# Optimization experiments

Hardware: AMD Instinct MI355X
Metric: run time of the kernel (lower is better)

Reference implementation:

```python
import jax, jax.numpy as jnp
import numpy as np

N_NODES = 50000
N_EDGES = 800000
IN_FEAT = 100
OUT_FEAT = 100
NUM_RELS = 200
NUM_HEADS = 3
NUM_BASES = 100
SUB_IN = 1   # in_feat // num_bases
SUB_OUT = 1  # out_feat // num_bases


def setup_inputs() -> dict:
    key = jax.random.key(0)
    ks = jax.random.split(key, 10)
    return {
        "h": jax.random.normal(ks[0], (N_NODES, IN_FEAT), jnp.float32),
        "e": jax.random.normal(ks[1], (N_EDGES, IN_FEAT), jnp.float32),
        "norm": jax.random.uniform(ks[2], (N_NODES, 1), jnp.float32),
        "weight": jax.random.normal(ks[3], (NUM_RELS, NUM_BASES * SUB_IN * SUB_OUT), jnp.float32) * 0.1,
        "attn": jax.random.normal(ks[4], (NUM_RELS, NUM_HEADS, OUT_FEAT), jnp.float32) * 0.1,
        "fc_w": jax.random.normal(ks[5], (IN_FEAT, OUT_FEAT * NUM_HEADS), jnp.float32) * 0.1,
        "loop_w": jax.random.normal(ks[6], (IN_FEAT, OUT_FEAT), jnp.float32) * 0.1,
        "rel": jax.random.randint(ks[7], (N_EDGES,), 0, NUM_RELS, jnp.int32),
        "src": jax.random.randint(ks[8], (N_EDGES,), 0, N_NODES, jnp.int32),
        "dst": jax.random.randint(ks[9], (N_EDGES,), 0, N_NODES, jnp.int32),
    }


def reference(h, e, norm, weight, attn, fc_w, loop_w, rel, src, dst):
    E = rel.shape[0]
    # --- relation-indexed block-diagonal message (torch.bmm over blocks) ---
    W_e = weight[rel].reshape(E, NUM_BASES, SUB_IN, SUB_OUT)        # per-edge block weights
    h_src = h[src].reshape(E, NUM_BASES, SUB_IN)                    # gathered src features
    msg = jnp.einsum('ebi,ebio->ebo', h_src, W_e).reshape(E, OUT_FEAT)
    # --- edge-feature attention fuse ---
    a_e = attn[rel]                                                 # (E, H, OUT)
    fc_e = (e @ fc_w).reshape(E, NUM_HEADS, OUT_FEAT)               # fc(edge)
    feat = jax.nn.leaky_relu(a_e * fc_e, 0.2).sum(axis=1)           # (E, OUT)
    msg = msg + feat
    # --- scatter-sum aggregation to dst nodes, then norm + self-loop ---
    agg = jax.ops.segment_sum(msg, dst, num_segments=N_NODES)       # (N, OUT)
    node = agg * norm
    loop_message = h @ loop_w
    return node + loop_message
```

## Files before the change

### kernel.cpp

```cpp
#include <hip/hip_runtime.h>
#include <hip/hip_bf16.h>

#define N_NODES 50000
#define N_EDGES 800000
#define IN_FEAT 100
#define OUT_FEAT 100
#define NUM_RELS 200
#define NUM_HEADS 3

#define KP 128
#define NPH 112
#define NP  336
#define MB  128
#define NT_O 7

#define WS_B       0u
#define WS_LW      86016u
#define WS_CNT     114688u
#define WS_OFFS    315392u
#define WS_CURSOR  516096u
#define WS_BSUM    716800u
#define WS_PERM    717056u
#define WS_FEAT    3917056u
#define NNODES_PAD 50176

typedef __attribute__((ext_vector_type(8))) short short8;
typedef __attribute__((ext_vector_type(4))) float f32x4;

__device__ __forceinline__ unsigned short f2bf(float f) {
    unsigned u = __builtin_bit_cast(unsigned, f);
    unsigned r = u + 0x7FFFu + ((u >> 16) & 1u);
    return (unsigned short)(r >> 16);
}
__device__ __forceinline__ float bf2f(unsigned hs) {
    return __builtin_bit_cast(float, hs << 16);
}

__global__ __launch_bounds__(256) void build_B(const float* __restrict__ fc_w,
                                               unsigned short* __restrict__ Bws) {
    int idx = blockIdx.x * 256 + threadIdx.x;
    if (idx >= NP * 16) return;
    int n = idx >> 4, g = idx & 15;
    int head = n / NPH, nl = n - head * NPH;
    int kt = g >> 2, g4 = g & 3;
    unsigned p[4];
#pragma unroll
    for (int half = 0; half < 2; ++half) {
#pragma unroll
        for (int jp = 0; jp < 2; ++jp) {
            int k_lo = kt * 32 + half * 16 + g4 * 4 + jp * 2;
            int k_hi = k_lo + 1;
            float vlo = (k_lo < IN_FEAT && nl < OUT_FEAT)
                      ? fc_w[k_lo * (OUT_FEAT * NUM_HEADS) + head * OUT_FEAT + nl] : 0.f;
            float vhi = (k_hi < IN_FEAT && nl < OUT_FEAT)
                      ? fc_w[k_hi * (OUT_FEAT * NUM_HEADS) + head * OUT_FEAT + nl] : 0.f;
            p[half * 2 + jp] = (unsigned)f2bf(vlo) | ((unsigned)f2bf(vhi) << 16);
        }
    }
    unsigned off = (unsigned)(head * (NPH * KP * 2)) +
                   (((unsigned)(nl * (KP * 2) + g * 16)) ^ (((unsigned)(nl & 7)) << 4));
    *reinterpret_cast<int4*>(reinterpret_cast<char*>(Bws) + off) =
        make_int4((int)p[0], (int)p[1], (int)p[2], (int)p[3]);
}

__global__ __launch_bounds__(256) void build_LW(const float* __restrict__ loop_w,
                                                unsigned short* __restrict__ LWws) {
    int idx = blockIdx.x * 256 + threadIdx.x;
    if (idx >= NPH * 16) return;
    int nl = idx >> 4, g = idx & 15;
    int kt = g >> 2, g4 = g & 3;
    unsigned p[4];
#pragma unroll
    for (int half = 0; half < 2; ++half) {
#pragma unroll
        for (int jp = 0; jp < 2; ++jp) {
            int k_lo = kt * 32 + half * 16 + g4 * 4 + jp * 2;
            int k_hi = k_lo + 1;
            float vlo = (k_lo < IN_FEAT && nl < OUT_FEAT) ? loop_w[k_lo * OUT_FEAT + nl] : 0.f;
            float vhi = (k_hi < IN_FEAT && nl < OUT_FEAT) ? loop_w[k_hi * OUT_FEAT + nl] : 0.f;
            p[half * 2 + jp] = (unsigned)f2bf(vlo) | ((unsigned)f2bf(vhi) << 16);
        }
    }
    unsigned off = ((unsigned)(nl * (KP * 2) + g * 16)) ^ (((unsigned)(nl & 7)) << 4);
    *reinterpret_cast<int4*>(reinterpret_cast<char*>(LWws) + off) =
        make_int4((int)p[0], (int)p[1], (int)p[2], (int)p[3]);
}

__global__ __launch_bounds__(512, 2) void loop_gemm(const float* __restrict__ h,
                                                    const unsigned short* __restrict__ LWimg,
                                                    float* __restrict__ out) {
    __shared__ unsigned short Alds[MB * KP];
    __shared__ unsigned short Blds[NPH * KP];
    const int tid = threadIdx.x;
    const int rbase = blockIdx.x * MB;

    {
        const int4* sp = reinterpret_cast<const int4*>(LWimg);
        int4* dp = reinterpret_cast<int4*>(Blds);
        for (int i = tid; i < NPH * KP / 8; i += 512) dp[i] = sp[i];
    }
    for (int gi = tid; gi < MB * 16; gi += 512) {
        int row = gi >> 4, g = gi & 15;
        int grow = rbase + row;
        int kt = g >> 2, g4 = g & 3;
        const float* hrow = h + (size_t)grow * IN_FEAT;
        int k0 = kt * 32 + g4 * 4, k1 = k0 + 16;
        bool ok = grow < N_NODES;
        float4 va = (ok && k0 + 4 <= IN_FEAT) ? *reinterpret_cast<const float4*>(hrow + k0)
                                              : make_float4(0.f, 0.f, 0.f, 0.f);
        float4 vb = (ok && k1 + 4 <= IN_FEAT) ? *reinterpret_cast<const float4*>(hrow + k1)
                                              : make_float4(0.f, 0.f, 0.f, 0.f);
        unsigned p0 = (unsigned)f2bf(va.x) | ((unsigned)f2bf(va.y) << 16);
        unsigned p1 = (unsigned)f2bf(va.z) | ((unsigned)f2bf(va.w) << 16);
        unsigned p2 = (unsigned)f2bf(vb.x) | ((unsigned)f2bf(vb.y) << 16);
        unsigned p3 = (unsigned)f2bf(vb.z) | ((unsigned)f2bf(vb.w) << 16);
        unsigned off = ((unsigned)(row * (KP * 2) + g * 16)) ^ (((unsigned)(row & 7)) << 4);
        *reinterpret_cast<int4*>(reinterpret_cast<char*>(Alds) + off) =
            make_int4((int)p0, (int)p1, (int)p2, (int)p3);
    }
    __syncthreads();

    const int wave = tid >> 6, lane = tid & 63;
    const int lrow = lane & 15, lk = lane >> 4;
    const int arow = wave * 16 + lrow;
    const unsigned aswz = ((unsigned)(arow & 7)) << 4;
    const unsigned bswz = ((unsigned)(lrow & 7)) << 4;

    f32x4 acc[NT_O];
#pragma unroll
    for (int i = 0; i < NT_O; ++i) acc[i] = (f32x4){0.f, 0.f, 0.f, 0.f};

#pragma unroll
    for (int kt = 0; kt < 4; ++kt) {
        unsigned aoff = ((unsigned)(arow * (KP * 2) + kt * 64 + lk * 16)) ^ aswz;
        short8 afrag = *reinterpret_cast<const short8*>(
            reinterpret_cast<const char*>(Alds) + aoff);
#pragma unroll
        for (int nt = 0; nt < NT_O; ++nt) {
            unsigned boff = ((unsigned)((nt * 16 + lrow) * (KP * 2) + kt * 64 + lk * 16)) ^ bswz;
            short8 bfrag = *reinterpret_cast<const short8*>(
                reinterpret_cast<const char*>(Blds) + boff);
            acc[nt] = __builtin_amdgcn_mfma_f32_16x16x32_bf16(afrag, bfrag, acc[nt], 0, 0, 0);
        }
    }
#pragma unroll
    for (int nt = 0; nt < NT_O; ++nt) {
        int o = nt * 16 + lrow;
        if (o < OUT_FEAT) {
#pragma unroll
            for (int r = 0; r < 4; ++r) {
                int grow = rbase + wave * 16 + lk * 4 + r;
                if (grow < N_NODES) out[(size_t)grow * OUT_FEAT + o] = acc[nt][r];
            }
        }
    }
}

__global__ __launch_bounds__(512) void hist_kernel(const int* __restrict__ dst,
                                                   int* __restrict__ cnt) {
    int e = blockIdx.x * 512 + threadIdx.x;
    if (e < N_EDGES) atomicAdd(&cnt[dst[e]], 1);
}

__global__ __launch_bounds__(1024) void scan1(const int* __restrict__ cnt,
                                              int* __restrict__ offs,
                                              int* __restrict__ bsum) {
    __shared__ int s[1024];
    int i = blockIdx.x * 1024 + threadIdx.x;
    int v = (i < N_NODES) ? cnt[i] : 0;
    s[threadIdx.x] = v;
    __syncthreads();
    for (int d = 1; d < 1024; d <<= 1) {
        int t = (threadIdx.x >= d) ? s[threadIdx.x - d] : 0;
        __syncthreads();
        s[threadIdx.x] += t;
        __syncthreads();
    }
    offs[i] = s[threadIdx.x] - v;
    if (threadIdx.x == 1023) bsum[blockIdx.x] = s[1023];
}

__global__ __launch_bounds__(64) void scan2(int* __restrict__ bsum) {
    __shared__ int s[64];
    int v = (threadIdx.x < NNODES_PAD / 1024) ? bsum[threadIdx.x] : 0;
    s[threadIdx.x] = v;
    __syncthreads();
    for (int d = 1; d < 64; d <<= 1) {
        int t = (threadIdx.x >= d) ? s[threadIdx.x - d] : 0;
        __syncthreads();
        s[threadIdx.x] += t;
        __syncthreads();
    }
    bsum[threadIdx.x] = s[threadIdx.x] - v;
}

__global__ __launch_bounds__(1024) void scan3(int* __restrict__ offs,
                                              const int* __restrict__ bsum,
                                              int* __restrict__ cursor) {
    int i = blockIdx.x * 1024 + threadIdx.x;
    int v = offs[i] + bsum[blockIdx.x];
    offs[i] = v;
    cursor[i] = v;
}

__global__ __launch_bounds__(512) void scatter_kernel(const int* __restrict__ dst,
                                                      int* __restrict__ cursor,
                                                      int* __restrict__ perm) {
    int e = blockIdx.x * 512 + threadIdx.x;
    if (e < N_EDGES) {
        int p = atomicAdd(&cursor[dst[e]], 1);
        perm[p] = e;
    }
}

template<bool TOWS>
__global__ __launch_bounds__(512, 2) void feat_kernel(
        const float* __restrict__ efeat, const int* __restrict__ rel,
        const unsigned short* __restrict__ Bimg, const float* __restrict__ attn,
        const float* __restrict__ h, const float* __restrict__ weight,
        const float* __restrict__ norm, const int* __restrict__ src,
        const int* __restrict__ dst, float* __restrict__ out,
        unsigned short* __restrict__ featws, int lo) {

    __shared__ unsigned short Blds[NPH * KP];
    __shared__ int   m_rel[MB];
    __shared__ int   m_src[MB];
    __shared__ int   m_dst[MB];
    __shared__ float m_nrm[MB];

    const int tid = threadIdx.x;
    const int ebase = lo + blockIdx.x * MB;

    if (tid < MB) {
        int ei = ebase + tid;
        m_rel[tid] = rel[ei];
        if (!TOWS) {
            int d = dst[ei];
            m_src[tid] = src[ei]; m_dst[tid] = d; m_nrm[tid] = norm[d];
        }
    }

    const int wave = tid >> 6, lane = tid & 63;
    const int lrow = lane & 15, lk = lane >> 4;
    const int arow = ebase + wave * 16 + lrow;
    const float* ap = efeat + (size_t)arow * IN_FEAT;

    short8 afrag[4];
#pragma unroll
    for (int kt = 0; kt < 4; ++kt) {
        int k0 = kt * 32 + lk * 4;
        int k1 = k0 + 16;
        float4 va = (k0 + 4 <= IN_FEAT) ? *reinterpret_cast<const float4*>(ap + k0)
                                        : make_float4(0.f, 0.f, 0.f, 0.f);
        float4 vb = (k1 + 4 <= IN_FEAT) ? *reinterpret_cast<const float4*>(ap + k1)
                                        : make_float4(0.f, 0.f, 0.f, 0.f);
        afrag[kt][0] = (short)f2bf(va.x); afrag[kt][1] = (short)f2bf(va.y);
        afrag[kt][2] = (short)f2bf(va.z); afrag[kt][3] = (short)f2bf(va.w);
        afrag[kt][4] = (short)f2bf(vb.x); afrag[kt][5] = (short)f2bf(vb.y);
        afrag[kt][6] = (short)f2bf(vb.z); afrag[kt][7] = (short)f2bf(vb.w);
    }

    const unsigned bswz = ((unsigned)(lrow & 7)) << 4;
    float feat[NT_O][4];
#pragma unroll
    for (int nt = 0; nt < NT_O; ++nt)
#pragma unroll
        for (int r = 0; r < 4; ++r) feat[nt][r] = 0.f;

    int rl_r[4];

    for (int hh = 0; hh < NUM_HEADS; ++hh) {
        {
            const int4* sp = reinterpret_cast<const int4*>(Bimg) + hh * (NPH * KP / 8);
            int4* dp = reinterpret_cast<int4*>(Blds);
            for (int i = tid; i < NPH * KP / 8; i += 512) dp[i] = sp[i];
        }
        __syncthreads();
        if (hh == 0) {
#pragma unroll
            for (int r = 0; r < 4; ++r) rl_r[r] = m_rel[wave * 16 + lk * 4 + r];
        }

        f32x4 acc[NT_O];
#pragma unroll
        for (int i = 0; i < NT_O; ++i) acc[i] = (f32x4){0.f, 0.f, 0.f, 0.f};

#pragma unroll
        for (int kt = 0; kt < 4; ++kt) {
#pragma unroll
            for (int nt = 0; nt < NT_O; ++nt) {
                unsigned boff = ((unsigned)((nt * 16 + lrow) * (KP * 2) + kt * 64 + lk * 16)) ^ bswz;
                short8 bfrag = *reinterpret_cast<const short8*>(
                    reinterpret_cast<const char*>(Blds) + boff);
                acc[nt] = __builtin_amdgcn_mfma_f32_16x16x32_bf16(afrag[kt], bfrag, acc[nt], 0, 0, 0);
            }
        }
#pragma unroll
        for (int nt = 0; nt < NT_O; ++nt) {
            int o = nt * 16 + lrow;
            if (o < OUT_FEAT) {
#pragma unroll
                for (int r = 0; r < 4; ++r) {
                    float v = acc[nt][r] *
                              attn[rl_r[r] * (NUM_HEADS * OUT_FEAT) + hh * OUT_FEAT + o];
                    feat[nt][r] += (v > 0.f) ? v : 0.2f * v;
                }
            }
        }
        __syncthreads();
    }

    if (TOWS) {
#pragma unroll
        for (int nt = 0; nt < NT_O; ++nt) {
            int o = nt * 16 + lrow;
            if (o < OUT_FEAT) {
#pragma unroll
                for (int r = 0; r < 4; ++r) {
                    int el = wave * 16 + lk * 4 + r;
                    Blds[el * NPH + o] = f2bf(feat[nt][r]);
                }
            }
        }
        __syncthreads();
        int4* gp = reinterpret_cast<int4*>(featws + (size_t)(ebase - lo) * NPH);
        const int4* sp = reinterpret_cast<const int4*>(Blds);
        for (int i = tid; i < MB * NPH / 8; i += 512) gp[i] = sp[i];
    } else {
#pragma unroll
        for (int nt = 0; nt < NT_O; ++nt) {
            int o = nt * 16 + lrow;
            if (o < OUT_FEAT) {
#pragma unroll
                for (int r = 0; r < 4; ++r) {
                    int el = wave * 16 + lk * 4 + r;
                    float mg = h[(size_t)m_src[el] * IN_FEAT + o] * weight[rl_r[r] * OUT_FEAT + o];
                    atomicAdd(&out[(size_t)m_dst[el] * OUT_FEAT + o],
                              (mg + feat[nt][r]) * m_nrm[el]);
                }
            }
        }
    }
}

__global__ __launch_bounds__(256, 4) void agg_kernel(
        const unsigned short* __restrict__ featws, const int* __restrict__ offs,
        const int* __restrict__ cnt, const int* __restrict__ perm,
        const int* __restrict__ src, const int* __restrict__ rel,
        const float* __restrict__ h, const float* __restrict__ weight,
        const float* __restrict__ norm, float* __restrict__ out,
        int lo, int hi) {
    int wv = threadIdx.x >> 6, lane = threadIdx.x & 63;
    int n = blockIdx.x * 4 + wv;
    if (n >= N_NODES) return;
    int start = offs[n], deg = cnt[n];
    const int c = lane;
    float ax = 0.f, ay = 0.f;
    const unsigned* fp = reinterpret_cast<const unsigned*>(featws);

    for (int base = 0; base < deg; base += 64) {
        int rem = deg - base; if (rem > 64) rem = 64;
        int ev = 0, sv = 0, rv = 0;
        if (lane < rem) {
            ev = perm[start + base + lane];
            sv = src[ev];
            rv = rel[ev];
        }
#pragma unroll 1
        for (int j = 0; j < rem; ++j) {
            int e = __shfl(ev, j);
            if (e < lo || e >= hi) continue;
            int s = __shfl(sv, j);
            int rl = __shfl(rv, j);
            if (c < OUT_FEAT / 2) {
                float2 h2 = *reinterpret_cast<const float2*>(h + (size_t)s * IN_FEAT + 2 * c);
                float2 w2 = *reinterpret_cast<const float2*>(weight + (size_t)rl * OUT_FEAT + 2 * c);
                unsigned fu = fp[(size_t)(e - lo) * (NPH / 2) + c];
                ax += h2.x * w2.x + bf2f(fu & 0xffffu);
                ay += h2.y * w2.y + bf2f(fu >> 16);
            }
        }
    }
    if (c < OUT_FEAT / 2 && deg > 0) {
        float nm = norm[n];
        float2* op = reinterpret_cast<float2*>(out + (size_t)n * OUT_FEAT) + c;
        float2 cur = *op;
        cur.x += ax * nm; cur.y += ay * nm;
        *op = cur;
    }
}

extern "C" void kernel_launch(void* const* d_in, const int* in_sizes, int n_in,
                              void* d_out, int out_size, void* d_ws, size_t ws_size,
                              hipStream_t stream) {
    const float* h      = (const float*)d_in[0];
    const float* efeat  = (const float*)d_in[1];
    const float* norm   = (const float*)d_in[2];
    const float* weight = (const float*)d_in[3];
    const float* attn   = (const float*)d_in[4];
    const float* fc_w   = (const float*)d_in[5];
    const float* loop_w = (const float*)d_in[6];
    const int*   rel    = (const int*)d_in[7];
    const int*   src    = (const int*)d_in[8];
    const int*   dst    = (const int*)d_in[9];
    float* out = (float*)d_out;

    char* ws = (char*)d_ws;
    unsigned short* Bimg  = (unsigned short*)(ws + WS_B);
    unsigned short* LWimg = (unsigned short*)(ws + WS_LW);
    int* cnt    = (int*)(ws + WS_CNT);
    int* offs   = (int*)(ws + WS_OFFS);
    int* cursor = (int*)(ws + WS_CURSOR);
    int* bsum   = (int*)(ws + WS_BSUM);
    int* perm   = (int*)(ws + WS_PERM);
    unsigned short* featws = (unsigned short*)(ws + WS_FEAT);

    build_B<<<(NP * 16 + 255) / 256, 256, 0, stream>>>(fc_w, Bimg);
    build_LW<<<(NPH * 16 + 255) / 256, 256, 0, stream>>>(loop_w, LWimg);
    loop_gemm<<<(N_NODES + MB - 1) / MB, 512, 0, stream>>>(h, LWimg, out);

    long long avail = (long long)ws_size - (long long)WS_FEAT;
    long long rows = (avail > 0) ? avail / (NPH * 2) : 0;
    rows = (rows / MB) * MB;
    if (rows > N_EDGES) rows = N_EDGES;

    if (rows >= 100000) {
        hipMemsetAsync(cnt, 0, NNODES_PAD * sizeof(int), stream);
        hist_kernel<<<(N_EDGES + 511) / 512, 512, 0, stream>>>(dst, cnt);
        scan1<<<NNODES_PAD / 1024, 1024, 0, stream>>>(cnt, offs, bsum);
        scan2<<<1, 64, 0, stream>>>(bsum);
        scan3<<<NNODES_PAD / 1024, 1024, 0, stream>>>(offs, bsum, cursor);
        scatter_kernel<<<(N_EDGES + 511) / 512, 512, 0, stream>>>(dst, cursor, perm);

        for (long long lo = 0; lo < N_EDGES; lo += rows) {
            long long hi = lo + rows; if (hi > N_EDGES) hi = N_EDGES;
            int nb = (int)((hi - lo) / MB);
            feat_kernel<true><<<nb, 512, 0, stream>>>(
                efeat, rel, Bimg, attn, h, weight, norm, src, dst, out,
                featws, (int)lo);
            agg_kernel<<<(N_NODES + 3) / 4, 256, 0, stream>>>(
                featws, offs, cnt, perm, src, rel, h, weight, norm, out,
                (int)lo, (int)hi);
        }
    } else {
        feat_kernel<false><<<N_EDGES / MB, 512, 0, stream>>>(
            efeat, rel, Bimg, attn, h, weight, norm, src, dst, out,
            featws, 0);
    }
}
```

Before: 485.8 us.

## Read MFMA B fragments directly from global memory, drop LDS staging and block barriers

```diff
diff --git a/kernel.cpp b/kernel.cpp
--- a/kernel.cpp
+++ b/kernel.cpp
@@ -57,10 +57,7 @@
             p[half * 2 + jp] = (unsigned)f2bf(vlo) | ((unsigned)f2bf(vhi) << 16);
         }
     }
-    unsigned off = (unsigned)(head * (NPH * KP * 2)) +
-                   (((unsigned)(nl * (KP * 2) + g * 16)) ^ (((unsigned)(nl & 7)) << 4));
-    *reinterpret_cast<int4*>(reinterpret_cast<char*>(Bws) + off) =
-        make_int4((int)p[0], (int)p[1], (int)p[2], (int)p[3]);
+    reinterpret_cast<int4*>(Bws)[idx] = make_int4((int)p[0], (int)p[1], (int)p[2], (int)p[3]);
 }
 
 __global__ __launch_bounds__(256) void build_LW(const float* __restrict__ loop_w,
@@ -81,76 +78,49 @@
             p[half * 2 + jp] = (unsigned)f2bf(vlo) | ((unsigned)f2bf(vhi) << 16);
         }
     }
-    unsigned off = ((unsigned)(nl * (KP * 2) + g * 16)) ^ (((unsigned)(nl & 7)) << 4);
-    *reinterpret_cast<int4*>(reinterpret_cast<char*>(LWws) + off) =
-        make_int4((int)p[0], (int)p[1], (int)p[2], (int)p[3]);
+    reinterpret_cast<int4*>(LWws)[idx] = make_int4((int)p[0], (int)p[1], (int)p[2], (int)p[3]);
 }
 
 __global__ __launch_bounds__(512, 2) void loop_gemm(const float* __restrict__ h,
                                                     const unsigned short* __restrict__ LWimg,
                                                     float* __restrict__ out) {
-    __shared__ unsigned short Alds[MB * KP];
-    __shared__ unsigned short Blds[NPH * KP];
     const int tid = threadIdx.x;
-    const int rbase = blockIdx.x * MB;
-
-    {
-        const int4* sp = reinterpret_cast<const int4*>(LWimg);
-        int4* dp = reinterpret_cast<int4*>(Blds);
-        for (int i = tid; i < NPH * KP / 8; i += 512) dp[i] = sp[i];
-    }
-    for (int gi = tid; gi < MB * 16; gi += 512) {
-        int row = gi >> 4, g = gi & 15;
-        int grow = rbase + row;
-        int kt = g >> 2, g4 = g & 3;
-        const float* hrow = h + (size_t)grow * IN_FEAT;
-        int k0 = kt * 32 + g4 * 4, k1 = k0 + 16;
-        bool ok = grow < N_NODES;
-        float4 va = (ok && k0 + 4 <= IN_FEAT) ? *reinterpret_cast<const float4*>(hrow + k0)
-                                              : make_float4(0.f, 0.f, 0.f, 0.f);
-        float4 vb = (ok && k1 + 4 <= IN_FEAT) ? *reinterpret_cast<const float4*>(hrow + k1)
-                                              : make_float4(0.f, 0.f, 0.f, 0.f);
-        unsigned p0 = (unsigned)f2bf(va.x) | ((unsigned)f2bf(va.y) << 16);
-        unsigned p1 = (unsigned)f2bf(va.z) | ((unsigned)f2bf(va.w) << 16);
-        unsigned p2 = (unsigned)f2bf(vb.x) | ((unsigned)f2bf(vb.y) << 16);
-        unsigned p3 = (unsigned)f2bf(vb.z) | ((unsigned)f2bf(vb.w) << 16);
-        unsigned off = ((unsigned)(row * (KP * 2) + g * 16)) ^ (((unsigned)(row & 7)) << 4);
-        *reinterpret_cast<int4*>(reinterpret_cast<char*>(Alds) + off) =
-            make_int4((int)p0, (int)p1, (int)p2, (int)p3);
-    }
-    __syncthreads();
-
     const int wave = tid >> 6, lane = tid & 63;
     const int lrow = lane & 15, lk = lane >> 4;
-    const int arow = wave * 16 + lrow;
-    const unsigned aswz = ((unsigned)(arow & 7)) << 4;
-    const unsigned bswz = ((unsigned)(lrow & 7)) << 4;
-
-    f32x4 acc[NT_O];
-#pragma unroll
-    for (int i = 0; i < NT_O; ++i) acc[i] = (f32x4){0.f, 0.f, 0.f, 0.f};
-
+    const int rbase = blockIdx.x * MB;
+    const int grow = rbase + wave * 16 + lrow;
+    const bool ok = grow < N_NODES;
+    const float* ap = h + (size_t)grow * IN_FEAT;
+
+    short8 afrag[4];
 #pragma unroll
     for (int kt = 0; kt < 4; ++kt) {
-        unsigned aoff = ((unsigned)(arow * (KP * 2) + kt * 64 + lk * 16)) ^ aswz;
-        short8 afrag = *reinterpret_cast<const short8*>(
-            reinterpret_cast<const char*>(Alds) + aoff);
-#pragma unroll
-        for (int nt = 0; nt < NT_O; ++nt) {
-            unsigned boff = ((unsigned)((nt * 16 + lrow) * (KP * 2) + kt * 64 + lk * 16)) ^ bswz;
+        int k0 = kt * 32 + lk * 4, k1 = k0 + 16;
+        float4 va = (ok && k0 + 4 <= IN_FEAT) ? *reinterpret_cast<const float4*>(ap + k0)
+                                              : make_float4(0.f, 0.f, 0.f, 0.f);
+        float4 vb = (ok && k1 + 4 <= IN_FEAT) ? *reinterpret_cast<const float4*>(ap + k1)
+                                              : make_float4(0.f, 0.f, 0.f, 0.f);
+        afrag[kt][0] = (short)f2bf(va.x); afrag[kt][1] = (short)f2bf(va.y);
+        afrag[kt][2] = (short)f2bf(va.z); afrag[kt][3] = (short)f2bf(va.w);
+        afrag[kt][4] = (short)f2bf(vb.x); afrag[kt][5] = (short)f2bf(vb.y);
+        afrag[kt][6] = (short)f2bf(vb.z); afrag[kt][7] = (short)f2bf(vb.w);
+    }
+
+#pragma unroll
+    for (int nt = 0; nt < NT_O; ++nt) {
+        f32x4 acc = (f32x4){0.f, 0.f, 0.f, 0.f};
+#pragma unroll
+        for (int kt = 0; kt < 4; ++kt) {
             short8 bfrag = *reinterpret_cast<const short8*>(
-                reinterpret_cast<const char*>(Blds) + boff);
-            acc[nt] = __builtin_amdgcn_mfma_f32_16x16x32_bf16(afrag, bfrag, acc[nt], 0, 0, 0);
-        }
-    }
-#pragma unroll
-    for (int nt = 0; nt < NT_O; ++nt) {
+                LWimg + ((nt * 16 + lrow) * KP + kt * 32 + lk * 8));
+            acc = __builtin_amdgcn_mfma_f32_16x16x32_bf16(afrag[kt], bfrag, acc, 0, 0, 0);
+        }
         int o = nt * 16 + lrow;
         if (o < OUT_FEAT) {
 #pragma unroll
             for (int r = 0; r < 4; ++r) {
-                int grow = rbase + wave * 16 + lk * 4 + r;
-                if (grow < N_NODES) out[(size_t)grow * OUT_FEAT + o] = acc[nt][r];
+                int crow = rbase + wave * 16 + lk * 4 + r;
+                if (crow < N_NODES) out[(size_t)crow * OUT_FEAT + o] = acc[r];
             }
         }
     }
@@ -222,34 +192,19 @@
         const int* __restrict__ dst, float* __restrict__ out,
         unsigned short* __restrict__ featws, int lo) {
 
-    __shared__ unsigned short Blds[NPH * KP];
-    __shared__ int   m_rel[MB];
-    __shared__ int   m_src[MB];
-    __shared__ int   m_dst[MB];
-    __shared__ float m_nrm[MB];
+    __shared__ unsigned short slice[8][16 * NPH];
 
     const int tid = threadIdx.x;
-    const int ebase = lo + blockIdx.x * MB;
-
-    if (tid < MB) {
-        int ei = ebase + tid;
-        m_rel[tid] = rel[ei];
-        if (!TOWS) {
-            int d = dst[ei];
-            m_src[tid] = src[ei]; m_dst[tid] = d; m_nrm[tid] = norm[d];
-        }
-    }
-
     const int wave = tid >> 6, lane = tid & 63;
     const int lrow = lane & 15, lk = lane >> 4;
+    const int ebase = lo + blockIdx.x * MB;
     const int arow = ebase + wave * 16 + lrow;
     const float* ap = efeat + (size_t)arow * IN_FEAT;
 
     short8 afrag[4];
 #pragma unroll
     for (int kt = 0; kt < 4; ++kt) {
-        int k0 = kt * 32 + lk * 4;
-        int k1 = k0 + 16;
+        int k0 = kt * 32 + lk * 4, k1 = k0 + 16;
         float4 va = (k0 + 4 <= IN_FEAT) ? *reinterpret_cast<const float4*>(ap + k0)
                                         : make_float4(0.f, 0.f, 0.f, 0.f);
         float4 vb = (k1 + 4 <= IN_FEAT) ? *reinterpret_cast<const float4*>(ap + k1)
@@ -260,40 +215,64 @@
         afrag[kt][6] = (short)f2bf(vb.z); afrag[kt][7] = (short)f2bf(vb.w);
     }
 
-    const unsigned bswz = ((unsigned)(lrow & 7)) << 4;
+    const float* at_r[4];
+#pragma unroll
+    for (int r = 0; r < 4; ++r)
+        at_r[r] = attn + (size_t)rel[ebase + wave * 16 + lk * 4 + r] * (NUM_HEADS * OUT_FEAT);
+
     float feat[NT_O][4];
 #pragma unroll
     for (int nt = 0; nt < NT_O; ++nt)
 #pragma unroll
         for (int r = 0; r < 4; ++r) feat[nt][r] = 0.f;
 
-    int rl_r[4];
-
+#pragma unroll 1
     for (int hh = 0; hh < NUM_HEADS; ++hh) {
-        {
-            const int4* sp = reinterpret_cast<const int4*>(Bimg) + hh * (NPH * KP / 8);
-            int4* dp = reinterpret_cast<int4*>(Blds);
-            for (int i = tid; i < NPH * KP / 8; i += 512) dp[i] = sp[i];
-        }
-        __syncthreads();
-        if (hh == 0) {
-#pragma unroll
-            for (int r = 0; r < 4; ++r) rl_r[r] = m_rel[wave * 16 + lk * 4 + r];
-        }
-
-        f32x4 acc[NT_O];
-#pragma unroll
-        for (int i = 0; i < NT_O; ++i) acc[i] = (f32x4){0.f, 0.f, 0.f, 0.f};
-
-#pragma unroll
-        for (int kt = 0; kt < 4; ++kt) {
-#pragma unroll
-            for (int nt = 0; nt < NT_O; ++nt) {
-                unsigned boff = ((unsigned)((nt * 16 + lrow) * (KP * 2) + kt * 64 + lk * 16)) ^ bswz;
+        const unsigned short* Bh = Bimg + (size_t)hh * (NPH * KP);
+#pragma unroll
+        for (int nt = 0; nt < NT_O; ++nt) {
+            f32x4 acc = (f32x4){0.f, 0.f, 0.f, 0.f};
+#pragma unroll
+            for (int kt = 0; kt < 4; ++kt) {
                 short8 bfrag = *reinterpret_cast<const short8*>(
-                    reinterpret_cast<const char*>(Blds) + boff);
-                acc[nt] = __builtin_amdgcn_mfma_f32_16x16x32_bf16(afrag[kt], bfrag, acc[nt], 0, 0, 0);
-            }
+                    Bh + ((nt * 16 + lrow) * KP + kt * 32 + lk * 8));
+                acc = __builtin_amdgcn_mfma_f32_16x16x32_bf16(afrag[kt], bfrag, acc, 0, 0, 0);
+            }
+            int o = nt * 16 + lrow;
+            if (o < OUT_FEAT) {
+                int oo = hh * OUT_FEAT + o;
+#pragma unroll
+                for (int r = 0; r < 4; ++r) {
+                    float v = acc[r] * at_r[r][oo];
+                    feat[nt][r] += (v > 0.f) ? v : 0.2f * v;
+                }
+            }
+        }
+    }
+
+    if (TOWS) {
+        unsigned short* sl = slice[wave];
+#pragma unroll
+        for (int nt = 0; nt < NT_O; ++nt) {
+            int o = nt * 16 + lrow;
+#pragma unroll
+            for (int r = 0; r < 4; ++r)
+                sl[(lk * 4 + r) * NPH + o] = f2bf(feat[nt][r]);
+        }
+        asm volatile("s_waitcnt lgkmcnt(0)" ::: "memory");
+        __builtin_amdgcn_sched_barrier(0);
+        const int4* sp = reinterpret_cast<const int4*>(sl);
+        int4* gp = reinterpret_cast<int4*>(featws + (size_t)(ebase - lo + wave * 16) * NPH);
+        gp[lane]       = sp[lane];
+        gp[lane + 64]  = sp[lane + 64];
+        gp[lane + 128] = sp[lane + 128];
+        if (lane < 32) gp[lane + 192] = sp[lane + 192];
+    } else {
+        int sr_r[4], d_r[4]; float nm_r[4];
+#pragma unroll
+        for (int r = 0; r < 4; ++r) {
+            int ei = ebase + wave * 16 + lk * 4 + r;
+            sr_r[r] = src[ei]; d_r[r] = dst[ei]; nm_r[r] = norm[d_r[r]];
         }
 #pragma unroll
         for (int nt = 0; nt < NT_O; ++nt) {
@@ -301,42 +280,11 @@
             if (o < OUT_FEAT) {
 #pragma unroll
                 for (int r = 0; r < 4; ++r) {
-                    float v = acc[nt][r] *
-                              attn[rl_r[r] * (NUM_HEADS * OUT_FEAT) + hh * OUT_FEAT + o];
-                    feat[nt][r] += (v > 0.f) ? v : 0.2f * v;
-                }
-            }
-        }
-        __syncthreads();
-    }
-
-    if (TOWS) {
-#pragma unroll
-        for (int nt = 0; nt < NT_O; ++nt) {
-            int o = nt * 16 + lrow;
-            if (o < OUT_FEAT) {
-#pragma unroll
-                for (int r = 0; r < 4; ++r) {
-                    int el = wave * 16 + lk * 4 + r;
-                    Blds[el * NPH + o] = f2bf(feat[nt][r]);
-                }
-            }
-        }
-        __syncthreads();
-        int4* gp = reinterpret_cast<int4*>(featws + (size_t)(ebase - lo) * NPH);
-        const int4* sp = reinterpret_cast<const int4*>(Blds);
-        for (int i = tid; i < MB * NPH / 8; i += 512) gp[i] = sp[i];
-    } else {
-#pragma unroll
-        for (int nt = 0; nt < NT_O; ++nt) {
-            int o = nt * 16 + lrow;
-            if (o < OUT_FEAT) {
-#pragma unroll
-                for (int r = 0; r < 4; ++r) {
-                    int el = wave * 16 + lk * 4 + r;
-                    float mg = h[(size_t)m_src[el] * IN_FEAT + o] * weight[rl_r[r] * OUT_FEAT + o];
-                    atomicAdd(&out[(size_t)m_dst[el] * OUT_FEAT + o],
-                              (mg + feat[nt][r]) * m_nrm[el]);
+                    const float* wr = weight +
+                        (size_t)((at_r[r] - attn) / (NUM_HEADS * OUT_FEAT)) * OUT_FEAT;
+                    float mg = h[(size_t)sr_r[r] * IN_FEAT + o] * wr[o];
+                    atomicAdd(&out[(size_t)d_r[r] * OUT_FEAT + o],
+                              (mg + feat[nt][r]) * nm_r[r]);
                 }
             }
         }
@@ -357,6 +305,7 @@
     const int c = lane;
     float ax = 0.f, ay = 0.f;
     const unsigned* fp = reinterpret_cast<const unsigned*>(featws);
+    const bool act = (c < OUT_FEAT / 2);
 
     for (int base = 0; base < deg; base += 64) {
         int rem = deg - base; if (rem > 64) rem = 64;
@@ -366,22 +315,48 @@
             sv = src[ev];
             rv = rel[ev];
         }
-#pragma unroll 1
-        for (int j = 0; j < rem; ++j) {
-            int e = __shfl(ev, j);
-            if (e < lo || e >= hi) continue;
-            int s = __shfl(sv, j);
-            int rl = __shfl(rv, j);
-            if (c < OUT_FEAT / 2) {
-                float2 h2 = *reinterpret_cast<const float2*>(h + (size_t)s * IN_FEAT + 2 * c);
-                float2 w2 = *reinterpret_cast<const float2*>(weight + (size_t)rl * OUT_FEAT + 2 * c);
-                unsigned fu = fp[(size_t)(e - lo) * (NPH / 2) + c];
-                ax += h2.x * w2.x + bf2f(fu & 0xffffu);
-                ay += h2.y * w2.y + bf2f(fu >> 16);
-            }
-        }
-    }
-    if (c < OUT_FEAT / 2 && deg > 0) {
+        int j = 0;
+        for (; j + 2 <= rem; j += 2) {
+            int e0 = __shfl(ev, j),     e1 = __shfl(ev, j + 1);
+            int s0 = __shfl(sv, j),     s1 = __shfl(sv, j + 1);
+            int r0 = __shfl(rv, j),     r1 = __shfl(rv, j + 1);
+            bool in0 = (e0 >= lo && e0 < hi), in1 = (e1 >= lo && e1 < hi);
+            if (act) {
+                float2 h0, w0, h1, w1; unsigned f0 = 0, f1 = 0;
+                if (in0) {
+                    h0 = *reinterpret_cast<const float2*>(h + (size_t)s0 * IN_FEAT + 2 * c);
+                    w0 = *reinterpret_cast<const float2*>(weight + (size_t)r0 * OUT_FEAT + 2 * c);
+                    f0 = fp[(size_t)(e0 - lo) * (NPH / 2) + c];
+                }
+                if (in1) {
+                    h1 = *reinterpret_cast<const float2*>(h + (size_t)s1 * IN_FEAT + 2 * c);
+                    w1 = *reinterpret_cast<const float2*>(weight + (size_t)r1 * OUT_FEAT + 2 * c);
+                    f1 = fp[(size_t)(e1 - lo) * (NPH / 2) + c];
+                }
+                if (in0) {
+                    ax += h0.x * w0.x + bf2f(f0 & 0xffffu);
+                    ay += h0.y * w0.y + bf2f(f0 >> 16);
+                }
+                if (in1) {
+                    ax += h1.x * w1.x + bf2f(f1 & 0xffffu);
+                    ay += h1.y * w1.y + bf2f(f1 >> 16);
+                }
+            }
+        }
+        if (j < rem) {
+            int e0 = __shfl(ev, j);
+            int s0 = __shfl(sv, j);
+            int r0 = __shfl(rv, j);
+            if (act && e0 >= lo && e0 < hi) {
+                float2 h0 = *reinterpret_cast<const float2*>(h + (size_t)s0 * IN_FEAT + 2 * c);
+                float2 w0 = *reinterpret_cast<const float2*>(weight + (size_t)r0 * OUT_FEAT + 2 * c);
+                unsigned f0 = fp[(size_t)(e0 - lo) * (NPH / 2) + c];
+                ax += h0.x * w0.x + bf2f(f0 & 0xffffu);
+                ay += h0.y * w0.y + bf2f(f0 >> 16);
+            }
+        }
+    }
+    if (act && deg > 0) {
         float nm = norm[n];
         float2* op = reinterpret_cast<float2*>(out + (size_t)n * OUT_FEAT) + c;
         float2 cur = *op;
```

New measurement: 778.4 us. 1.6x slower.
